# Kernel tuning notes

Hardware: AMD Instinct MI355X
Metric: run time of the kernel (lower is better)

The kernel has to match this reference:

```python
import jax, jax.numpy as jnp
import numpy as np

EPS = 1e-6
SCALE = 0.125
CELL = 0.5
GRID_H = 4.0


def _grid_sample(img, grid):
    # img [B,C,H,W], grid [B,G1,G2,2] in [-1,1]; bilinear, zeros padding, align_corners=False
    B, C, H, W = img.shape
    x = (grid[..., 0] + 1.0) * (W * 0.5) - 0.5
    y = (grid[..., 1] + 1.0) * (H * 0.5) - 0.5
    x0 = jnp.floor(x)
    y0 = jnp.floor(y)
    wx = x - x0
    wy = y - y0
    b = jnp.arange(B)[:, None, None]

    def tap(xi, yi, wgt):
        valid = (xi >= 0) & (xi < W) & (yi >= 0) & (yi < H)
        xc = jnp.clip(xi, 0, W - 1).astype(jnp.int32)
        yc = jnp.clip(yi, 0, H - 1).astype(jnp.int32)
        v = img[b, :, yc, xc]  # [B,G1,G2,C]
        return v * (wgt * valid)[..., None]

    out = (tap(x0, y0, (1 - wx) * (1 - wy)) + tap(x0 + 1, y0, wx * (1 - wy))
           + tap(x0, y0 + 1, (1 - wx) * wy) + tap(x0 + 1, y0 + 1, wx * wy))
    return out.transpose(0, 3, 1, 2)  # [B,C,G1,G2]


def _forward(features, calib, grid, w, bias):
    B, C, Hf, Wf = features.shape
    yv = jnp.arange(0.0, GRID_H, CELL, dtype=features.dtype) - GRID_H / 2.0  # [ny+1]
    yc = jnp.stack([jnp.zeros_like(yv), yv, jnp.zeros_like(yv)], axis=-1)    # [ny+1,3] = (0,y,0)
    corners = grid[:, None] + yc[None, :, None, None, :]                     # [B,ny+1,D+1,W+1,3]
    # perspective projection: homog = calib[:, :3] @ p + calib[:, 3]; img = xy / z
    homog = jnp.einsum('bij,bydwj->bydwi', calib[:, :, :3], corners) + calib[:, None, None, None, :, 3]
    img_corners = homog[..., :2] / homog[..., 2:3]
    img_size = jnp.array([Wf, Hf], dtype=features.dtype) / SCALE
    nc = jnp.clip(2.0 * img_corners / img_size - 1.0, -1.0, 1.0)             # [B,ny+1,D+1,W+1,2]
    mins = jnp.minimum(nc[:, :-1, :-1, :-1], nc[:, :-1, 1:, :-1])
    maxs = jnp.maximum(nc[:, 1:, 1:, 1:], nc[:, 1:, :-1, 1:])
    bbox = jnp.concatenate([mins, maxs], axis=-1)                            # [B,ny,D,W,4]
    _, ny, D, Wd, _ = bbox.shape
    bbox = bbox.reshape(B, ny, D * Wd, 4)
    area = ((bbox[..., 2] - bbox[..., 0]) * (bbox[..., 3] - bbox[..., 1]) * (Hf * Wf * 0.25) + EPS)[:, None]
    visible = (area > EPS).astype(features.dtype)
    ii = jnp.cumsum(jnp.cumsum(features, axis=-1), axis=-2)                  # integral image [B,C,Hf,Wf]
    g_tl = bbox[..., jnp.array([0, 1])]
    g_br = bbox[..., jnp.array([2, 3])]
    g_tr = bbox[..., jnp.array([2, 1])]
    g_bl = bbox[..., jnp.array([0, 3])]
    vox = (_grid_sample(ii, g_tl) + _grid_sample(ii, g_br)
           - _grid_sample(ii, g_tr) - _grid_sample(ii, g_bl))                # [B,C,ny,D*W]
    vox = vox / area * visible
    vox = vox.transpose(0, 3, 1, 2).reshape(B * D * Wd, C * ny)             # [B*D*W, C*ny]
    ortho = (vox @ w.T + bias).reshape(B, D, Wd, -1)
    ortho = jax.nn.relu(ortho.transpose(0, 3, 1, 2))                         # [B,C,D,W]
    return ortho, ii, g_tl, g_br, g_tr, g_bl


def setup_inputs():
    key = jax.random.key(0)
    k1, k2, k3 = jax.random.split(key, 3)
    B, C, HF, WF, NG = 2, 256, 96, 320, 128
    ny = int(GRID_H / CELL) - 1  # 7 voxel cells
    features = jax.random.normal(k1, (B, C, HF, WF), dtype=jnp.float32)
    fx = 700.0
    cx = WF / SCALE / 2.0
    cy = HF / SCALE / 2.0
    calib = jnp.tile(jnp.array([[fx, 0.0, cx, 0.0],
                                [0.0, fx, cy, 0.0],
                                [0.0, 0.0, 1.0, 0.0]], dtype=jnp.float32), (B, 1, 1))
    xs = jnp.linspace(-32.0, 32.0, NG + 1)
    zs = jnp.linspace(1.0, 65.0, NG + 1)
    zz, xx = jnp.meshgrid(zs, xs, indexing='ij')
    grid = jnp.tile(jnp.stack([xx, jnp.zeros_like(xx), zz], axis=-1)[None], (B, 1, 1, 1)).astype(jnp.float32)
    w = jax.random.normal(k2, (C, ny * C), dtype=jnp.float32) * 0.02
    bias = jax.random.normal(k3, (C,), dtype=jnp.float32) * 0.02
    return {"features": features, "calib": calib, "grid": grid, "w": w, "bias": bias}


def reference(features, calib, grid, w, bias):
    return _forward(features, calib, grid, w, bias)
```

## Files before the change

kernel.cpp:

```cpp
#include <hip/hip_runtime.h>
#include <hip/hip_fp16.h>

typedef unsigned short ushort_t;
typedef __attribute__((ext_vector_type(8))) short short8;
typedef __attribute__((ext_vector_type(4))) float f32x4;

#define BB   2
#define CCH  256
#define HF   96
#define WF   320
#define NYC  7
#define DWT  16384
#define PLANE (HF*WF)
#define KDIM (CCH*NYC)
#define NKT  56
#define MS   8
#define POS_TOTAL (BB*DWT)

#define WBF_BYTES  ((size_t)16*NKT*64*8*2)
#define IITH_BYTES ((size_t)BB*PLANE*CCH*2)

__device__ __forceinline__ ushort_t f2bf(float f) {
    unsigned u = __float_as_uint(f);
    u += 0x7fffu + ((u >> 16) & 1u);
    return (ushort_t)(u >> 16);
}

__global__ __launch_bounds__(512)
void k_integral(const float* __restrict__ f, float* __restrict__ ii) {
    __shared__ float pl[PLANE];
    int bc = blockIdx.x;
    const float* src = f  + (size_t)bc * PLANE;
    float*       dst = ii + (size_t)bc * PLANE;
    int t = threadIdx.x;

    #pragma unroll
    for (int i = 0; i < PLANE / 4 / 512; ++i) {
        int idx = t + i * 512;
        reinterpret_cast<float4*>(pl)[idx] = reinterpret_cast<const float4*>(src)[idx];
    }
    __syncthreads();

    int lane = t & 63, wv = t >> 6;
    for (int rr = 0; rr < 12; ++rr) {
        float* row = &pl[(wv * 12 + rr) * WF];
        float v0 = row[lane * 5 + 0];
        float v1 = row[lane * 5 + 1];
        float v2 = row[lane * 5 + 2];
        float v3 = row[lane * 5 + 3];
        float v4 = row[lane * 5 + 4];
        v1 += v0; v2 += v1; v3 += v2; v4 += v3;
        float s = v4;
        #pragma unroll
        for (int d = 1; d < 64; d <<= 1) {
            float o = __shfl_up(s, d);
            if (lane >= d) s += o;
        }
        float pre = s - v4;
        row[lane * 5 + 0] = v0 + pre;
        row[lane * 5 + 1] = v1 + pre;
        row[lane * 5 + 2] = v2 + pre;
        row[lane * 5 + 3] = v3 + pre;
        row[lane * 5 + 4] = v4 + pre;
    }
    __syncthreads();

    if (t < WF) {
        int x = t;
        float acc = 0.f;
        #pragma unroll 4
        for (int y = 0; y < HF; ++y) {
            acc += pl[y * WF + x];
            dst[(size_t)y * WF + x] = acc;
        }
    }
}

__global__ void k_transpose(const float* __restrict__ ii, _Float16* __restrict__ iith) {
    __shared__ float tile[32][33];
    int x0 = blockIdx.x * 32;
    int c0 = blockIdx.y * 32;
    int by = blockIdx.z;
    int b  = by / HF;
    int y  = by % HF;
    const float* src = ii + (size_t)b * CCH * PLANE + (size_t)y * WF;
    unsigned* dstu = reinterpret_cast<unsigned*>(iith + (size_t)by * WF * CCH);
    int tx = threadIdx.x;
    int ty = threadIdx.y;
    #pragma unroll
    for (int i = 0; i < 4; ++i) {
        int c = c0 + ty + 8 * i;
        tile[ty + 8 * i][tx] = src[(size_t)c * PLANE + x0 + tx];
    }
    __syncthreads();
    int id = ty * 32 + tx;
    #pragma unroll
    for (int it = 0; it < 2; ++it) {
        int idx = it * 256 + id;
        int xl = idx >> 4;
        int j  = idx & 15;
        float f0 = tile[2 * j][xl];
        float f1 = tile[2 * j + 1][xl];
        __half2 hh = __floats2half2_rn(f0, f1);
        dstu[((size_t)(x0 + xl) * CCH + c0) / 2 + j] = *reinterpret_cast<unsigned*>(&hh);
    }
}

__global__ void k_geom(const float* __restrict__ calib, const float* __restrict__ grid,
                       float* __restrict__ gtl, float* __restrict__ gbr,
                       float* __restrict__ gtr, float* __restrict__ gbl) {
    int t = blockIdx.x * blockDim.x + threadIdx.x;
    if (t >= BB * NYC * DWT) return;
    int dw = t % DWT;
    int by = t / DWT;
    int y  = by % NYC;
    int b  = by / NYC;
    int d  = dw >> 7;
    int w  = dw & 127;
    const float* cb = calib + b * 12;

    float c0=cb[0],c1=cb[1],c2=cb[2],c3=cb[3];
    float c4=cb[4],c5=cb[5],c6=cb[6],c7=cb[7];
    float c8=cb[8],c9=cb[9],c10=cb[10],c11=cb[11];

    auto ncp = [&](int yy, int i, int j, float& ox, float& oy) {
        const float* g = grid + (((size_t)b * 129 + i) * 129 + j) * 3;
        float gx = g[0];
        float gy = g[1] + (0.5f * (float)yy - 2.0f);
        float gz = g[2];
        float h0 = c0*gx + c1*gy + c2*gz + c3;
        float h1 = c4*gx + c5*gy + c6*gz + c7;
        float h2 = c8*gx + c9*gy + c10*gz + c11;
        float ix = h0 / h2;
        float iy = h1 / h2;
        float nx = 2.0f * ix / ((float)WF / 0.125f) - 1.0f;
        float ny = 2.0f * iy / ((float)HF / 0.125f) - 1.0f;
        ox = fminf(fmaxf(nx, -1.f), 1.f);
        oy = fminf(fmaxf(ny, -1.f), 1.f);
    };

    float ax, ay, bx, byy, mx1, my1, mx2, my2;
    ncp(y,     d,     w,     ax,  ay);
    ncp(y,     d + 1, w,     bx,  byy);
    float minx = fminf(ax, bx), miny = fminf(ay, byy);
    ncp(y + 1, d + 1, w + 1, mx1, my1);
    ncp(y + 1, d,     w + 1, mx2, my2);
    float maxx = fmaxf(mx1, mx2), maxy = fmaxf(my1, my2);

    size_t o = (size_t)t * 2;
    gtl[o] = minx; gtl[o + 1] = miny;
    gbr[o] = maxx; gbr[o + 1] = maxy;
    gtr[o] = maxx; gtr[o + 1] = miny;
    gbl[o] = minx; gbl[o + 1] = maxy;
}

__global__ void k_prepack(const float* __restrict__ w, ushort_t* __restrict__ wbf) {
    int t = blockIdx.x * blockDim.x + threadIdx.x;
    if (t >= 16 * NKT * 64) return;
    int lane = t & 63;
    int kt   = (t >> 6) % NKT;
    int nt   = t / (NKT * 64);
    int r = lane & 15, g = lane >> 4;
    const float* wr = w + (size_t)(nt * 16 + r) * KDIM;
    ushort_t* dst = wbf + (size_t)t * 8;
    #pragma unroll
    for (int j = 0; j < 8; ++j) {
        int k  = kt * 32 + g * 8 + j;
        int yy = k >> 8;
        int cc = k & 255;
        dst[j] = f2bf(wr[cc * NYC + yy]);
    }
}

__global__ __launch_bounds__(256)
void k_sample(const _Float16* __restrict__ iith, const float* __restrict__ gtl,
              const float* __restrict__ gbr, ushort_t* __restrict__ voxf, int pos_base) {
    __shared__ int2 taps[MS][NYC][16];
    int t = threadIdx.x;
    int bid = blockIdx.x;
    int cpx = gridDim.x >> 3;
    int swz = (bid & 7) * cpx + (bid >> 3);
    int lpos0 = swz * MS;
    int pos0  = pos_base + lpos0;
    int b   = pos0 / DWT;
    int dw0 = pos0 % DWT;

    if (t < MS * NYC) {
        int p = t / NYC, y = t % NYC;
        size_t gi = (((size_t)(b * NYC + y)) * DWT + dw0 + p) * 2;
        float g0 = gtl[gi], g1 = gtl[gi + 1];
        float g2 = gbr[gi], g3 = gbr[gi + 1];
        float area = (g2 - g0) * (g3 - g1) * ((float)HF * (float)WF * 0.25f) + 1e-6f;
        float inv  = (area > 1e-6f) ? (1.0f / area) : 0.0f;
        const float sgn[4] = {1.f, 1.f, -1.f, -1.f};
        float px[4] = {g0, g2, g2, g0};
        float py[4] = {g1, g3, g1, g3};
        #pragma unroll
        for (int q = 0; q < 4; ++q) {
            float x  = (px[q] + 1.0f) * ((float)WF * 0.5f) - 0.5f;
            float yy = (py[q] + 1.0f) * ((float)HF * 0.5f) - 0.5f;
            float x0f = floorf(x), y0f = floorf(yy);
            float wx = x - x0f, wy = yy - y0f;
            float wq[4] = {(1.f-wx)*(1.f-wy), wx*(1.f-wy), (1.f-wx)*wy, wx*wy};
            #pragma unroll
            for (int s = 0; s < 4; ++s) {
                float xi = x0f + (float)(s & 1);
                float yi = y0f + (float)(s >> 1);
                bool valid = (xi >= 0.f) && (xi < (float)WF) && (yi >= 0.f) && (yi < (float)HF);
                int xc = (int)fminf(fmaxf(xi, 0.f), (float)(WF - 1));
                int yc = (int)fminf(fmaxf(yi, 0.f), (float)(HF - 1));
                taps[p][y][q * 4 + s] =
                    make_int2(yc * WF + xc, __float_as_int(valid ? (wq[s] * sgn[q] * inv) : 0.0f));
            }
        }
    }
    __syncthreads();

    int p = t >> 5;
    int c = (t & 31) * 8;
    int lpos = lpos0 + p;
    int mt = lpos >> 4, r = lpos & 15, g = (c >> 3) & 3;
    const _Float16* base = iith + (size_t)b * PLANE * CCH + c;
    ushort_t* vbase = voxf + ((size_t)mt * NKT * 64 + (size_t)(g * 16 + r)) * 8;

    for (int y = 0; y < NYC; ++y) {
        float acc[8] = {0.f,0.f,0.f,0.f,0.f,0.f,0.f,0.f};
        #pragma unroll
        for (int q = 0; q < 16; ++q) {
            int2 tp = taps[p][y][q];
            float wg = __int_as_float(tp.y);
            uint4 hv = *reinterpret_cast<const uint4*>(base + (size_t)tp.x * CCH);
            float2 f;
            f = __half22float2(*reinterpret_cast<__half2*>(&hv.x)); acc[0] += wg*f.x; acc[1] += wg*f.y;
            f = __half22float2(*reinterpret_cast<__half2*>(&hv.y)); acc[2] += wg*f.x; acc[3] += wg*f.y;
            f = __half22float2(*reinterpret_cast<__half2*>(&hv.z)); acc[4] += wg*f.x; acc[5] += wg*f.y;
            f = __half22float2(*reinterpret_cast<__half2*>(&hv.w)); acc[6] += wg*f.x; acc[7] += wg*f.y;
        }
        int kt = (y << 3) + (c >> 5);
        short8 o;
        #pragma unroll
        for (int j = 0; j < 8; ++j) o[j] = (short)f2bf(acc[j]);
        *reinterpret_cast<short8*>(vbase + (size_t)kt * 64 * 8) = o;
    }
}

__global__ __launch_bounds__(256)
void k_gemm(const ushort_t* __restrict__ voxf, const ushort_t* __restrict__ wbf,
            const float* __restrict__ bias, float* __restrict__ ortho, int pos_base) {
    int t = threadIdx.x;
    int lane = t & 63, wv = t >> 6;
    int mi = wv >> 1, ni = wv & 1;
    int bx = blockIdx.x;
    int swz = (bx & 7) * (gridDim.x >> 3) + (bx >> 3);
    int nhalf = swz & 1, pm = swz >> 1;
    int lpos0 = pm * 128;
    int pos0 = pos_base + lpos0;
    int b = pos0 / DWT, dw0 = pos0 % DWT;
    int mt0 = (lpos0 >> 4) + mi * 4;
    int nt0 = nhalf * 8 + ni * 4;

    const short8* ap = reinterpret_cast<const short8*>(voxf) + (size_t)mt0 * NKT * 64 + lane;
    const short8* bp = reinterpret_cast<const short8*>(wbf)  + (size_t)nt0 * NKT * 64 + lane;
    const size_t TS = (size_t)NKT * 64;

    f32x4 acc[4][4] = {};
    short8 A0[4], B0[4], A1[4], B1[4];
    #pragma unroll
    for (int i = 0; i < 4; ++i) {
        A0[i] = ap[i * TS];
        B0[i] = bp[i * TS];
        A1[i] = ap[i * TS + 64];
        B1[i] = bp[i * TS + 64];
    }

    for (int kt = 0; kt < NKT; kt += 2) {
        #pragma unroll
        for (int m = 0; m < 4; ++m)
            #pragma unroll
            for (int n = 0; n < 4; ++n)
                acc[m][n] = __builtin_amdgcn_mfma_f32_16x16x32_bf16(A0[m], B0[n], acc[m][n], 0, 0, 0);
        if (kt + 2 < NKT) {
            #pragma unroll
            for (int i = 0; i < 4; ++i) {
                A0[i] = ap[i * TS + (size_t)(kt + 2) * 64];
                B0[i] = bp[i * TS + (size_t)(kt + 2) * 64];
            }
        }
        #pragma unroll
        for (int m = 0; m < 4; ++m)
            #pragma unroll
            for (int n = 0; n < 4; ++n)
                acc[m][n] = __builtin_amdgcn_mfma_f32_16x16x32_bf16(A1[m], B1[n], acc[m][n], 0, 0, 0);
        if (kt + 3 < NKT) {
            #pragma unroll
            for (int i = 0; i < 4; ++i) {
                A1[i] = ap[i * TS + (size_t)(kt + 3) * 64];
                B1[i] = bp[i * TS + (size_t)(kt + 3) * 64];
            }
        }
    }

    int r = lane & 15, gq = lane >> 4;
    #pragma unroll
    for (int n = 0; n < 4; ++n) {
        int co = nhalf * 128 + (ni * 4 + n) * 16 + r;
        float bv = bias[co];
        float* ob = ortho + ((size_t)(b * CCH + co)) * DWT + dw0 + gq * 4;
        #pragma unroll
        for (int m = 0; m < 4; ++m) {
            float4 o = make_float4(fmaxf(acc[m][n][0] + bv, 0.f), fmaxf(acc[m][n][1] + bv, 0.f),
                                   fmaxf(acc[m][n][2] + bv, 0.f), fmaxf(acc[m][n][3] + bv, 0.f));
            *reinterpret_cast<float4*>(ob + (mi * 4 + m) * 16) = o;
        }
    }
}

extern "C" void kernel_launch(void* const* d_in, const int* in_sizes, int n_in,
                              void* d_out, int out_size, void* d_ws, size_t ws_size,
                              hipStream_t stream) {
    const float* features = (const float*)d_in[0];
    const float* calib    = (const float*)d_in[1];
    const float* grid     = (const float*)d_in[2];
    const float* w        = (const float*)d_in[3];
    const float* bias     = (const float*)d_in[4];

    float* out   = (float*)d_out;
    float* ortho = out;
    float* ii    = out + (size_t)8388608;
    float* gtl   = out + (size_t)24117248;
    float* gbr   = out + (size_t)24576000;
    float* gtr   = out + (size_t)25034752;
    float* gbl   = out + (size_t)25493504;

    ushort_t* wbf  = (ushort_t*)d_ws;
    _Float16* iith = (_Float16*)((char*)d_ws + WBF_BYTES);
    ushort_t* voxf = (ushort_t*)((char*)d_ws + WBF_BYTES + IITH_BYTES);

    k_integral<<<BB * CCH, 512, 0, stream>>>(features, ii);
    k_geom    <<<(BB * NYC * DWT + 255) / 256, 256, 0, stream>>>(calib, grid, gtl, gbr, gtr, gbl);
    k_prepack <<<(16 * NKT * 64 + 255) / 256, 256, 0, stream>>>(w, wbf);
    dim3 gT(WF / 32, CCH / 32, BB * HF);
    k_transpose<<<gT, dim3(32, 8), 0, stream>>>(ii, iith);

    size_t vox_all = (size_t)POS_TOTAL * KDIM * 2;
    int nch = (ws_size >= WBF_BYTES + IITH_BYTES + vox_all) ? 1 : 4;
    int cpos = POS_TOTAL / nch;
    for (int cidx = 0; cidx < nch; ++cidx) {
        int pb = cidx * cpos;
        k_sample<<<cpos / MS, 256, 0, stream>>>(iith, gtl, gbr, voxf, pb);
        k_gemm  <<<(cpos / 128) * 2, 256, 0, stream>>>(voxf, wbf, bias, ortho, pb);
    }
}
```

Measured before the change: 179.0 us.

## Fuse box-sampling and projection GEMM into one kernel with fp16 MFMA

Merges the separate sampling and GEMM kernels into a single kernel. Each wave computes the box-filtered voxel features for 16 positions and feeds them straight into fp16 MFMAs against prepacked fp16 weights, with no voxel-feature buffer in global memory. This removes the write and re-read of the large intermediate and one launch per chunk. Weights switch from bf16 to fp16. The cost is that each block re-streams the whole weight matrix from cache, holds 16 accumulator tiles per wave, and interleaves gather latency with MFMA work.

```diff
diff --git a/kernel.cpp b/kernel.cpp
--- a/kernel.cpp
+++ b/kernel.cpp
@@ -2,7 +2,7 @@
 #include <hip/hip_fp16.h>
 
 typedef unsigned short ushort_t;
-typedef __attribute__((ext_vector_type(8))) short short8;
+typedef __attribute__((ext_vector_type(8))) _Float16 f16x8;
 typedef __attribute__((ext_vector_type(4))) float f32x4;
 
 #define BB   2
@@ -14,17 +14,11 @@
 #define PLANE (HF*WF)
 #define KDIM (CCH*NYC)
 #define NKT  56
-#define MS   8
+#define MB   128
 #define POS_TOTAL (BB*DWT)
 
-#define WBF_BYTES  ((size_t)16*NKT*64*8*2)
+#define WH_BYTES   ((size_t)NKT*16*64*8*2)
 #define IITH_BYTES ((size_t)BB*PLANE*CCH*2)
-
-__device__ __forceinline__ ushort_t f2bf(float f) {
-    unsigned u = __float_as_uint(f);
-    u += 0x7fffu + ((u >> 16) & 1u);
-    return (ushort_t)(u >> 16);
-}
 
 __global__ __launch_bounds__(512)
 void k_integral(const float* __restrict__ f, float* __restrict__ ii) {
@@ -154,39 +148,39 @@
     gbl[o] = minx; gbl[o + 1] = maxy;
 }
 
-__global__ void k_prepack(const float* __restrict__ w, ushort_t* __restrict__ wbf) {
+__global__ void k_prepack(const float* __restrict__ w, _Float16* __restrict__ wh) {
     int t = blockIdx.x * blockDim.x + threadIdx.x;
-    if (t >= 16 * NKT * 64) return;
+    if (t >= NKT * 16 * 64) return;
     int lane = t & 63;
-    int kt   = (t >> 6) % NKT;
-    int nt   = t / (NKT * 64);
+    int nt   = (t >> 6) & 15;
+    int kt   = t >> 10;
     int r = lane & 15, g = lane >> 4;
     const float* wr = w + (size_t)(nt * 16 + r) * KDIM;
-    ushort_t* dst = wbf + (size_t)t * 8;
+    _Float16* dst = wh + (size_t)t * 8;
     #pragma unroll
     for (int j = 0; j < 8; ++j) {
         int k  = kt * 32 + g * 8 + j;
         int yy = k >> 8;
         int cc = k & 255;
-        dst[j] = f2bf(wr[cc * NYC + yy]);
-    }
-}
-
-__global__ __launch_bounds__(256)
-void k_sample(const _Float16* __restrict__ iith, const float* __restrict__ gtl,
-              const float* __restrict__ gbr, ushort_t* __restrict__ voxf, int pos_base) {
-    __shared__ int2 taps[MS][NYC][16];
+        dst[j] = (_Float16)wr[cc * NYC + yy];
+    }
+}
+
+__global__ __launch_bounds__(512, 2)
+void k_fused(const _Float16* __restrict__ iith, const _Float16* __restrict__ wh,
+             const float* __restrict__ gtl, const float* __restrict__ gbr,
+             const float* __restrict__ bias, float* __restrict__ ortho) {
+    __shared__ int2 taps[MB][NYC][17];
+
     int t = threadIdx.x;
     int bid = blockIdx.x;
-    int cpx = gridDim.x >> 3;
-    int swz = (bid & 7) * cpx + (bid >> 3);
-    int lpos0 = swz * MS;
-    int pos0  = pos_base + lpos0;
+    int swz = (bid & 7) * (gridDim.x >> 3) + (bid >> 3);
+    int pos0 = swz * MB;
     int b   = pos0 / DWT;
     int dw0 = pos0 % DWT;
 
-    if (t < MS * NYC) {
-        int p = t / NYC, y = t % NYC;
+    for (int idx = t; idx < MB * NYC; idx += 512) {
+        int p = idx / NYC, y = idx % NYC;
         size_t gi = (((size_t)(b * NYC + y)) * DWT + dw0 + p) * 2;
         float g0 = gtl[gi], g1 = gtl[gi + 1];
         float g2 = gbr[gi], g3 = gbr[gi + 1];
@@ -216,102 +210,55 @@
     }
     __syncthreads();
 
-    int p = t >> 5;
-    int c = (t & 31) * 8;
-    int lpos = lpos0 + p;
-    int mt = lpos >> 4, r = lpos & 15, g = (c >> 3) & 3;
-    const _Float16* base = iith + (size_t)b * PLANE * CCH + c;
-    ushort_t* vbase = voxf + ((size_t)mt * NKT * 64 + (size_t)(g * 16 + r)) * 8;
+    int lane = t & 63, wv = t >> 6;
+    int r = lane & 15, g = lane >> 4;
+    int p = wv * 16 + r;
+    const _Float16* ibase = iith + (size_t)b * PLANE * CCH;
+    const f16x8*    bbase = reinterpret_cast<const f16x8*>(wh) + lane;
+
+    f32x4 acc[16] = {};
 
     for (int y = 0; y < NYC; ++y) {
-        float acc[8] = {0.f,0.f,0.f,0.f,0.f,0.f,0.f,0.f};
-        #pragma unroll
-        for (int q = 0; q < 16; ++q) {
-            int2 tp = taps[p][y][q];
-            float wg = __int_as_float(tp.y);
-            uint4 hv = *reinterpret_cast<const uint4*>(base + (size_t)tp.x * CCH);
-            float2 f;
-            f = __half22float2(*reinterpret_cast<__half2*>(&hv.x)); acc[0] += wg*f.x; acc[1] += wg*f.y;
-            f = __half22float2(*reinterpret_cast<__half2*>(&hv.y)); acc[2] += wg*f.x; acc[3] += wg*f.y;
-            f = __half22float2(*reinterpret_cast<__half2*>(&hv.z)); acc[4] += wg*f.x; acc[5] += wg*f.y;
-            f = __half22float2(*reinterpret_cast<__half2*>(&hv.w)); acc[6] += wg*f.x; acc[7] += wg*f.y;
-        }
-        int kt = (y << 3) + (c >> 5);
-        short8 o;
-        #pragma unroll
-        for (int j = 0; j < 8; ++j) o[j] = (short)f2bf(acc[j]);
-        *reinterpret_cast<short8*>(vbase + (size_t)kt * 64 * 8) = o;
-    }
-}
-
-__global__ __launch_bounds__(256)
-void k_gemm(const ushort_t* __restrict__ voxf, const ushort_t* __restrict__ wbf,
-            const float* __restrict__ bias, float* __restrict__ ortho, int pos_base) {
-    int t = threadIdx.x;
-    int lane = t & 63, wv = t >> 6;
-    int mi = wv >> 1, ni = wv & 1;
-    int bx = blockIdx.x;
-    int swz = (bx & 7) * (gridDim.x >> 3) + (bx >> 3);
-    int nhalf = swz & 1, pm = swz >> 1;
-    int lpos0 = pm * 128;
-    int pos0 = pos_base + lpos0;
-    int b = pos0 / DWT, dw0 = pos0 % DWT;
-    int mt0 = (lpos0 >> 4) + mi * 4;
-    int nt0 = nhalf * 8 + ni * 4;
-
-    const short8* ap = reinterpret_cast<const short8*>(voxf) + (size_t)mt0 * NKT * 64 + lane;
-    const short8* bp = reinterpret_cast<const short8*>(wbf)  + (size_t)nt0 * NKT * 64 + lane;
-    const size_t TS = (size_t)NKT * 64;
-
-    f32x4 acc[4][4] = {};
-    short8 A0[4], B0[4], A1[4], B1[4];
-    #pragma unroll
-    for (int i = 0; i < 4; ++i) {
-        A0[i] = ap[i * TS];
-        B0[i] = bp[i * TS];
-        A1[i] = ap[i * TS + 64];
-        B1[i] = bp[i * TS + 64];
-    }
-
-    for (int kt = 0; kt < NKT; kt += 2) {
-        #pragma unroll
-        for (int m = 0; m < 4; ++m)
-            #pragma unroll
-            for (int n = 0; n < 4; ++n)
-                acc[m][n] = __builtin_amdgcn_mfma_f32_16x16x32_bf16(A0[m], B0[n], acc[m][n], 0, 0, 0);
-        if (kt + 2 < NKT) {
-            #pragma unroll
-            for (int i = 0; i < 4; ++i) {
-                A0[i] = ap[i * TS + (size_t)(kt + 2) * 64];
-                B0[i] = bp[i * TS + (size_t)(kt + 2) * 64];
+        int2 tp[16];
+        #pragma unroll
+        for (int q = 0; q < 16; ++q) tp[q] = taps[p][y][q];
+
+        #pragma unroll
+        for (int cc = 0; cc < 8; ++cc) {
+            int kt = y * 8 + cc;
+            int c0 = cc * 32 + g * 8;
+            float ps[8] = {0.f,0.f,0.f,0.f,0.f,0.f,0.f,0.f};
+            #pragma unroll
+            for (int q = 0; q < 16; ++q) {
+                float wg = __int_as_float(tp[q].y);
+                uint4 hv = *reinterpret_cast<const uint4*>(ibase + (size_t)tp[q].x * CCH + c0);
+                float2 f;
+                f = __half22float2(*reinterpret_cast<__half2*>(&hv.x)); ps[0] += wg*f.x; ps[1] += wg*f.y;
+                f = __half22float2(*reinterpret_cast<__half2*>(&hv.y)); ps[2] += wg*f.x; ps[3] += wg*f.y;
+                f = __half22float2(*reinterpret_cast<__half2*>(&hv.z)); ps[4] += wg*f.x; ps[5] += wg*f.y;
+                f = __half22float2(*reinterpret_cast<__half2*>(&hv.w)); ps[6] += wg*f.x; ps[7] += wg*f.y;
             }
-        }
-        #pragma unroll
-        for (int m = 0; m < 4; ++m)
-            #pragma unroll
-            for (int n = 0; n < 4; ++n)
-                acc[m][n] = __builtin_amdgcn_mfma_f32_16x16x32_bf16(A1[m], B1[n], acc[m][n], 0, 0, 0);
-        if (kt + 3 < NKT) {
-            #pragma unroll
-            for (int i = 0; i < 4; ++i) {
-                A1[i] = ap[i * TS + (size_t)(kt + 3) * 64];
-                B1[i] = bp[i * TS + (size_t)(kt + 3) * 64];
+            f16x8 a;
+            #pragma unroll
+            for (int j = 0; j < 8; ++j) a[j] = (_Float16)ps[j];
+
+            const f16x8* bp = bbase + (size_t)kt * 16 * 64;
+            #pragma unroll
+            for (int nt = 0; nt < 16; ++nt) {
+                f16x8 bf = bp[(size_t)nt * 64];
+                acc[nt] = __builtin_amdgcn_mfma_f32_16x16x32_f16(a, bf, acc[nt], 0, 0, 0);
             }
         }
     }
 
-    int r = lane & 15, gq = lane >> 4;
-    #pragma unroll
-    for (int n = 0; n < 4; ++n) {
-        int co = nhalf * 128 + (ni * 4 + n) * 16 + r;
+    #pragma unroll
+    for (int nt = 0; nt < 16; ++nt) {
+        int co = nt * 16 + r;
         float bv = bias[co];
-        float* ob = ortho + ((size_t)(b * CCH + co)) * DWT + dw0 + gq * 4;
-        #pragma unroll
-        for (int m = 0; m < 4; ++m) {
-            float4 o = make_float4(fmaxf(acc[m][n][0] + bv, 0.f), fmaxf(acc[m][n][1] + bv, 0.f),
-                                   fmaxf(acc[m][n][2] + bv, 0.f), fmaxf(acc[m][n][3] + bv, 0.f));
-            *reinterpret_cast<float4*>(ob + (mi * 4 + m) * 16) = o;
-        }
+        float* ob = ortho + ((size_t)(b * CCH + co)) * DWT + dw0 + wv * 16 + g * 4;
+        float4 o = make_float4(fmaxf(acc[nt][0] + bv, 0.f), fmaxf(acc[nt][1] + bv, 0.f),
+                               fmaxf(acc[nt][2] + bv, 0.f), fmaxf(acc[nt][3] + bv, 0.f));
+        *reinterpret_cast<float4*>(ob) = o;
     }
 }
 
@@ -332,22 +279,14 @@
     float* gtr   = out + (size_t)25034752;
     float* gbl   = out + (size_t)25493504;
 
-    ushort_t* wbf  = (ushort_t*)d_ws;
-    _Float16* iith = (_Float16*)((char*)d_ws + WBF_BYTES);
-    ushort_t* voxf = (ushort_t*)((char*)d_ws + WBF_BYTES + IITH_BYTES);
+    _Float16* wh   = (_Float16*)d_ws;
+    _Float16* iith = (_Float16*)((char*)d_ws + WH_BYTES);
 
     k_integral<<<BB * CCH, 512, 0, stream>>>(features, ii);
     k_geom    <<<(BB * NYC * DWT + 255) / 256, 256, 0, stream>>>(calib, grid, gtl, gbr, gtr, gbl);
-    k_prepack <<<(16 * NKT * 64 + 255) / 256, 256, 0, stream>>>(w, wbf);
+    k_prepack <<<(NKT * 16 * 64 + 255) / 256, 256, 0, stream>>>(w, wh);
     dim3 gT(WF / 32, CCH / 32, BB * HF);
     k_transpose<<<gT, dim3(32, 8), 0, stream>>>(ii, iith);
 
-    size_t vox_all = (size_t)POS_TOTAL * KDIM * 2;
-    int nch = (ws_size >= WBF_BYTES + IITH_BYTES + vox_all) ? 1 : 4;
-    int cpos = POS_TOTAL / nch;
-    for (int cidx = 0; cidx < nch; ++cidx) {
-        int pb = cidx * cpos;
-        k_sample<<<cpos / MS, 256, 0, stream>>>(iith, gtl, gbr, voxf, pb);
-        k_gemm  <<<(cpos / 128) * 2, 256, 0, stream>>>(voxf, wbf, bias, ortho, pb);
-    }
-}
+    k_fused<<<POS_TOTAL / MB, 512, 0, stream>>>(iith, wh, gtl, gbr, bias, ortho);
+}
```

After: 356.3 us. +99.1%, slower.
